# Kernel tuning notes

Hardware: AMD Instinct MI355X
Metric: run time of the kernel (lower is better)

## Reference

```python
import jax, jax.numpy as jnp
import numpy as np
import math

B, S, E = 4, 4096, 1024
NUM_HEADS = 16
D = E // NUM_HEADS  # attention_size = 64


def setup_inputs() -> dict:
    key = jax.random.key(0)
    ks = jax.random.split(key, 7)
    queries = jax.random.normal(ks[0], (B, S, E), dtype=jnp.float32)
    keys = jax.random.normal(ks[1], (B, S, E), dtype=jnp.float32)
    values = jax.random.normal(ks[2], (B, S, E), dtype=jnp.float32)
    mask = jax.random.randint(ks[3], (B, S, S), 0, 2).astype(bool)
    # nn.Linear(E, D, bias=False): weight [D, E], y = x @ W^T
    lim = 1.0 / math.sqrt(E)
    W_q = jax.random.uniform(ks[4], (D, E), jnp.float32, -lim, lim)
    W_k = jax.random.uniform(ks[5], (D, E), jnp.float32, -lim, lim)
    W_v = jax.random.uniform(ks[6], (D, E), jnp.float32, -lim, lim)
    return {"queries": queries, "keys": keys, "values": values, "mask": mask,
            "W_q": W_q, "W_k": W_k, "W_v": W_v}


def reference(queries, keys, values, mask, W_q, W_k, W_v):
    Q = jnp.einsum('bse,de->bsd', queries, W_q)  # [B,S,D]
    K = jnp.einsum('bse,de->bsd', keys, W_k)
    V = jnp.einsum('bse,de->bsd', values, W_v)
    norm = math.sqrt(D)
    scores = jnp.einsum('bqd,bkd->bqk', Q, K) / norm  # [B,S,S]
    scores = jnp.where(mask, jnp.float32(-1e20), scores)
    attn = jax.nn.softmax(scores, axis=2)
    return jnp.einsum('bqk,bkd->bqd', attn, V)  # [B,S,D]
```

## Files before the change

### kernel.cpp

```cpp
#include <hip/hip_runtime.h>
#include <hip/hip_bf16.h>
#include <math.h>

#define NB 4
#define NS 4096
#define NE 1024
#define ND 64

typedef short bf16x8 __attribute__((ext_vector_type(8)));
typedef float f32x4  __attribute__((ext_vector_type(4)));

__device__ unsigned short g_Wb[3 * ND * NE];
__device__ unsigned short g_Qp[NB * NS * ND];
__device__ unsigned short g_Kp[NB * NS * ND];
__device__ unsigned short g_Vt[NB * ND * NS];
__device__ int g_flag;

static __device__ inline unsigned short f2bf(float f) {
    __hip_bfloat16 h = __float2bfloat16(f);
    return *reinterpret_cast<unsigned short*>(&h);
}
static __device__ inline unsigned int f2bf2(float lo, float hi) {
    __hip_bfloat162 h = __float22bfloat162_rn(make_float2(lo, hi));
    return *reinterpret_cast<unsigned int*>(&h);
}
static __device__ inline float bf2f(short s) {
    return __uint_as_float(((unsigned int)(unsigned short)s) << 16);
}

#define AS1 __attribute__((address_space(1)))
#define AS3 __attribute__((address_space(3)))
static __device__ __forceinline__ void gll16(const void* g, void* l) {
    __builtin_amdgcn_global_load_lds((const AS1 void*)g, (AS3 void*)l, 16, 0, 0);
}

__global__ void detect_mask(const unsigned int* __restrict__ mw) {
    __shared__ int found;
    if (threadIdx.x == 0) found = 0;
    __syncthreads();
    int f = 0;
    for (int i = threadIdx.x; i < 4096; i += 256)
        if (mw[i] > 1u) f = 1;
    if (f) atomicOr(&found, 1);
    __syncthreads();
    if (threadIdx.x == 0) g_flag = found;
}

__global__ void prep_w(const float* __restrict__ Wq, const float* __restrict__ Wk,
                       const float* __restrict__ Wv) {
    const int z = blockIdx.x;
    const float* W = (z == 0) ? Wq : (z == 1) ? Wk : Wv;
    unsigned short* o = g_Wb + (size_t)z * (ND * NE);
    const float scale = (z == 0) ? 0.125f : 1.0f;
    int i0 = blockIdx.y * 2048 + threadIdx.x * 8;
    float4 a = *(const float4*)&W[i0];
    float4 b = *(const float4*)&W[i0 + 4];
    ushort4 u0 = { f2bf(a.x * scale), f2bf(a.y * scale), f2bf(a.z * scale), f2bf(a.w * scale) };
    ushort4 u1 = { f2bf(b.x * scale), f2bf(b.y * scale), f2bf(b.z * scale), f2bf(b.w * scale) };
    *(ushort4*)&o[i0]     = u0;
    *(ushort4*)&o[i0 + 4] = u1;
}

__global__ __launch_bounds__(256) void proj_kernel(
    const float* __restrict__ Xq, const float* __restrict__ Xk, const float* __restrict__ Xv)
{
    __shared__ unsigned short Xs[2][64][72];

    const int z = blockIdx.y;
    const float* X = (z == 0) ? Xq : (z == 1) ? Xk : Xv;
    const unsigned short* W = g_Wb + (size_t)z * (ND * NE);

    const int t    = threadIdx.x;
    const int wv   = t >> 6;
    const int lane = t & 63;
    const int quad = lane >> 4;
    const int l16  = lane & 15;
    const int m0   = blockIdx.x * 64;

    const int sr  = t >> 4;
    const int sc4 = (t & 15) * 4;
    const float* Xb = X + (size_t)m0 * NE;

    float4 xr[4][4];

    #pragma unroll
    for (int d = 0; d < 4; ++d)
        #pragma unroll
        for (int p = 0; p < 4; ++p)
            xr[d][p] = *(const float4*)&Xb[(size_t)(sr + p * 16) * NE + d * 64 + sc4];
    #pragma unroll
    for (int p = 0; p < 4; ++p) {
        uint2 u = { f2bf2(xr[0][p].x, xr[0][p].y), f2bf2(xr[0][p].z, xr[0][p].w) };
        *(uint2*)&Xs[0][sr + p * 16][sc4] = u;
    }
    __syncthreads();

    f32x4 acc[4] = {};

    #pragma unroll
    for (int c = 0; c < 16; ++c) {
        if (c + 4 < 16) {
            #pragma unroll
            for (int p = 0; p < 4; ++p)
                xr[c & 3][p] = *(const float4*)&Xb[(size_t)(sr + p * 16) * NE + (c + 4) * 64 + sc4];
        }

        #pragma unroll
        for (int ks = 0; ks < 2; ++ks) {
            bf16x8 a = *(const bf16x8*)&Xs[c & 1][wv * 16 + l16][ks * 32 + quad * 8];
            #pragma unroll
            for (int nt = 0; nt < 4; ++nt) {
                bf16x8 bb = *(const bf16x8*)&W[(size_t)(nt * 16 + l16) * NE + c * 64 + ks * 32 + quad * 8];
                acc[nt] = __builtin_amdgcn_mfma_f32_16x16x32_bf16(a, bb, acc[nt], 0, 0, 0);
            }
        }

        if (c + 1 < 16) {
            #pragma unroll
            for (int p = 0; p < 4; ++p) {
                float4 v = xr[(c + 1) & 3][p];
                uint2 u = { f2bf2(v.x, v.y), f2bf2(v.z, v.w) };
                *(uint2*)&Xs[(c + 1) & 1][sr + p * 16][sc4] = u;
            }
        }
        __syncthreads();
    }

    #pragma unroll
    for (int nt = 0; nt < 4; ++nt)
        #pragma unroll
        for (int r = 0; r < 4; ++r) {
            int m   = m0 + wv * 16 + quad * 4 + r;
            int col = nt * 16 + l16;
            unsigned short u = f2bf(acc[nt][r]);
            if (z == 0)      g_Qp[(size_t)m * ND + col] = u;
            else if (z == 1) g_Kp[(size_t)m * ND + col] = u;
            else             g_Vt[((size_t)(m >> 12) * ND + col) * NS + (m & 4095)] = u;
        }
}

__global__ __launch_bounds__(256) void attn_kernel(
    const void* __restrict__ maskp, float* __restrict__ out)
{
    __shared__ unsigned short KT[2][64 * 64];
    __shared__ unsigned short VT[2][64 * 64];
    __shared__ unsigned char  MR[4][4][1024];
    __shared__ short          Ss[4][16][72];

    const int t    = threadIdx.x;
    const int wv   = t >> 6;
    const int lane = t & 63;
    const int quad = lane >> 4;
    const int l16  = lane & 15;

    const int n    = blockIdx.x;
    const int xcd  = n & 7;
    const int b    = xcd >> 1;
    const int q0   = ((n >> 3) * 2 + (xcd & 1)) * 64;
    const int wq0  = q0 + wv * 16;

    const bool m_u8 = (g_flag != 0);
    const unsigned char* m8  = (const unsigned char*)maskp;
    const int*           m32 = (const int*)maskp;

    const unsigned short* Qrow = g_Qp + ((size_t)b * NS + wq0 + l16) * ND;
    const bf16x8 qf0 = *(const bf16x8*)&Qrow[quad * 8];
    const bf16x8 qf1 = *(const bf16x8*)&Qrow[32 + quad * 8];

    const unsigned short* Kbase = g_Kp + ((size_t)b * NS) * ND;
    const unsigned short* Vbase = g_Vt + (size_t)b * ND * NS;

    const int r8 = lane >> 3;
    const int c8 = lane & 7;
    const int sw = c8 ^ r8;

    const unsigned char* m8base =
        m8 + ((size_t)b * NS + wq0 + (lane >> 2)) * (size_t)NS + (lane & 3) * 16;

    float l_row = 0.0f;
    f32x4 Oacc[4] = {};

    const int rsw = l16 & 7;

    if (m_u8) {
        #pragma unroll
        for (int j = 0; j < 2; ++j) {
            const int row = wv * 16 + j * 8 + r8;
            gll16(Kbase + (size_t)row * 64 + sw * 8, &KT[0][(wv * 16 + j * 8) * 64]);
            gll16(Vbase + (size_t)row * 4096 + sw * 8, &VT[0][(wv * 16 + j * 8) * 64]);
        }
        gll16(m8base, &MR[0][wv][0]);
        gll16(m8base + 64, &MR[1][wv][0]);
        asm volatile("s_waitcnt vmcnt(1)" ::: "memory");
        __builtin_amdgcn_s_barrier();

        #pragma unroll 2
        for (int it = 0; it < 64; ++it) {
            const int buf = it & 1;
            const int k0  = it * 64;

            if (it < 63) {
                const int k1 = k0 + 64;
                #pragma unroll
                for (int j = 0; j < 2; ++j) {
                    const int row = wv * 16 + j * 8 + r8;
                    gll16(Kbase + (size_t)(k1 + row) * 64 + sw * 8,
                          &KT[buf ^ 1][(wv * 16 + j * 8) * 64]);
                    gll16(Vbase + (size_t)row * 4096 + k1 + sw * 8,
                          &VT[buf ^ 1][(wv * 16 + j * 8) * 64]);
                }
            }
            if (it < 62)
                gll16(m8base + (it + 2) * 64, &MR[(it + 2) & 3][wv][0]);

            f32x4 sc[4] = {};
            #pragma unroll
            for (int kt = 0; kt < 4; ++kt) {
                const int row = kt * 16 + l16;
                bf16x8 kf0 = *(const bf16x8*)&KT[buf][row * 64 + ((quad ^ rsw) << 3)];
                bf16x8 kf1 = *(const bf16x8*)&KT[buf][row * 64 + (((4 + quad) ^ rsw) << 3)];
                sc[kt] = __builtin_amdgcn_mfma_f32_16x16x32_bf16(qf0, kf0, sc[kt], 0, 0, 0);
                sc[kt] = __builtin_amdgcn_mfma_f32_16x16x32_bf16(qf1, kf1, sc[kt], 0, 0, 0);
            }

            #pragma unroll
            for (int kt = 0; kt < 4; ++kt)
                #pragma unroll
                for (int r = 0; r < 4; ++r)
                    Ss[wv][quad * 4 + r][kt * 16 + l16] = (short)f2bf(__expf(sc[kt][r]));

            asm volatile("s_waitcnt lgkmcnt(0)" ::: "memory");

            bf16x8 a0 = *(const bf16x8*)&Ss[wv][l16][quad * 8];
            bf16x8 a1 = *(const bf16x8*)&Ss[wv][l16][32 + quad * 8];
            {
                const unsigned char* MRt = &MR[it & 3][wv][0];
                uint2 mm0 = *(const uint2*)&MRt[l16 * 64 + quad * 8];
                uint2 mm1 = *(const uint2*)&MRt[l16 * 64 + 32 + quad * 8];
                #pragma unroll
                for (int j = 0; j < 4; ++j) {
                    a0[j]     = ((mm0.x >> (8 * j)) & 255u) ? (short)0 : a0[j];
                    a0[4 + j] = ((mm0.y >> (8 * j)) & 255u) ? (short)0 : a0[4 + j];
                    a1[j]     = ((mm1.x >> (8 * j)) & 255u) ? (short)0 : a1[j];
                    a1[4 + j] = ((mm1.y >> (8 * j)) & 255u) ? (short)0 : a1[4 + j];
                }
            }
            {
                float ls = 0.0f;
                #pragma unroll
                for (int j = 0; j < 8; ++j) ls += bf2f(a0[j]) + bf2f(a1[j]);
                l_row += ls;
            }
            #pragma unroll
            for (int nt = 0; nt < 4; ++nt) {
                const int row = nt * 16 + l16;
                bf16x8 vf0 = *(const bf16x8*)&VT[buf][row * 64 + ((quad ^ rsw) << 3)];
                bf16x8 vf1 = *(const bf16x8*)&VT[buf][row * 64 + (((4 + quad) ^ rsw) << 3)];
                Oacc[nt] = __builtin_amdgcn_mfma_f32_16x16x32_bf16(a0, vf0, Oacc[nt], 0, 0, 0);
                Oacc[nt] = __builtin_amdgcn_mfma_f32_16x16x32_bf16(a1, vf1, Oacc[nt], 0, 0, 0);
            }

            if (it < 63) {
                if (it < 62) asm volatile("s_waitcnt vmcnt(1)" ::: "memory");
                else         asm volatile("s_waitcnt vmcnt(0)" ::: "memory");
                __builtin_amdgcn_s_barrier();
            }
        }
    } else {
        #pragma unroll
        for (int j = 0; j < 2; ++j) {
            const int row = wv * 16 + j * 8 + r8;
            gll16(Kbase + (size_t)row * 64 + sw * 8, &KT[0][(wv * 16 + j * 8) * 64]);
            gll16(Vbase + (size_t)row * 4096 + sw * 8, &VT[0][(wv * 16 + j * 8) * 64]);
        }
        asm volatile("s_waitcnt vmcnt(0)" ::: "memory");
        __builtin_amdgcn_s_barrier();

        #pragma unroll 2
        for (int it = 0; it < 64; ++it) {
            const int buf = it & 1;
            const int k0  = it * 64;

            if (it < 63) {
                const int k1 = k0 + 64;
                #pragma unroll
                for (int j = 0; j < 2; ++j) {
                    const int row = wv * 16 + j * 8 + r8;
                    gll16(Kbase + (size_t)(k1 + row) * 64 + sw * 8,
                          &KT[buf ^ 1][(wv * 16 + j * 8) * 64]);
                    gll16(Vbase + (size_t)row * 4096 + k1 + sw * 8,
                          &VT[buf ^ 1][(wv * 16 + j * 8) * 64]);
                }
            }

            f32x4 sc[4] = {};
            #pragma unroll
            for (int kt = 0; kt < 4; ++kt) {
                const int row = kt * 16 + l16;
                bf16x8 kf0 = *(const bf16x8*)&KT[buf][row * 64 + ((quad ^ rsw) << 3)];
                bf16x8 kf1 = *(const bf16x8*)&KT[buf][row * 64 + (((4 + quad) ^ rsw) << 3)];
                sc[kt] = __builtin_amdgcn_mfma_f32_16x16x32_bf16(qf0, kf0, sc[kt], 0, 0, 0);
                sc[kt] = __builtin_amdgcn_mfma_f32_16x16x32_bf16(qf1, kf1, sc[kt], 0, 0, 0);
            }

            #pragma unroll
            for (int r = 0; r < 4; ++r) {
                size_t mrow = ((size_t)b * NS + (wq0 + quad * 4 + r)) * (size_t)NS + k0;
                #pragma unroll
                for (int kt = 0; kt < 4; ++kt) {
                    int mv = m32[mrow + kt * 16 + l16];
                    float p = mv ? 0.0f : __expf(sc[kt][r]);
                    Ss[wv][quad * 4 + r][kt * 16 + l16] = (short)f2bf(p);
                }
            }

            asm volatile("s_waitcnt lgkmcnt(0)" ::: "memory");

            bf16x8 a0 = *(const bf16x8*)&Ss[wv][l16][quad * 8];
            bf16x8 a1 = *(const bf16x8*)&Ss[wv][l16][32 + quad * 8];
            {
                float ls = 0.0f;
                #pragma unroll
                for (int j = 0; j < 8; ++j) ls += bf2f(a0[j]) + bf2f(a1[j]);
                l_row += ls;
            }
            #pragma unroll
            for (int nt = 0; nt < 4; ++nt) {
                const int row = nt * 16 + l16;
                bf16x8 vf0 = *(const bf16x8*)&VT[buf][row * 64 + ((quad ^ rsw) << 3)];
                bf16x8 vf1 = *(const bf16x8*)&VT[buf][row * 64 + (((4 + quad) ^ rsw) << 3)];
                Oacc[nt] = __builtin_amdgcn_mfma_f32_16x16x32_bf16(a0, vf0, Oacc[nt], 0, 0, 0);
                Oacc[nt] = __builtin_amdgcn_mfma_f32_16x16x32_bf16(a1, vf1, Oacc[nt], 0, 0, 0);
            }

            if (it < 63) {
                asm volatile("s_waitcnt vmcnt(0)" ::: "memory");
                __builtin_amdgcn_s_barrier();
            }
        }
    }

    l_row += __shfl_xor(l_row, 16);
    l_row += __shfl_xor(l_row, 32);
    const float inv = 1.0f / l_row;

    #pragma unroll
    for (int r = 0; r < 4; ++r) {
        const float invm = __shfl(inv, quad * 4 + r);
        const int m = wq0 + quad * 4 + r;
        #pragma unroll
        for (int nt = 0; nt < 4; ++nt)
            out[((size_t)b * NS + m) * ND + nt * 16 + l16] = Oacc[nt][r] * invm;
    }
}

extern "C" void kernel_launch(void* const* d_in, const int* in_sizes, int n_in,
                              void* d_out, int out_size, void* d_ws, size_t ws_size,
                              hipStream_t stream) {
    const float* queries = (const float*)d_in[0];
    const float* keys    = (const float*)d_in[1];
    const float* values  = (const float*)d_in[2];
    const void*  mask    = d_in[3];
    const float* Wq      = (const float*)d_in[4];
    const float* Wk      = (const float*)d_in[5];
    const float* Wv      = (const float*)d_in[6];
    float* out = (float*)d_out;

    hipLaunchKernelGGL(detect_mask, dim3(1), dim3(256), 0, stream,
                       (const unsigned int*)mask);
    hipLaunchKernelGGL(prep_w, dim3(3, 32), dim3(256), 0, stream, Wq, Wk, Wv);
    hipLaunchKernelGGL(proj_kernel, dim3((NB * NS) / 64, 3), dim3(256), 0, stream,
                       queries, keys, values);
    hipLaunchKernelGGL(attn_kernel, dim3(NS / 64 * NB), dim3(256), 0, stream,
                       mask, out);
}
```

Baseline: 583.3 us.

## Split attention keys across two blocks, add merge kernel, coalesce projection stores

The attention grid doubles to 512 blocks, each handling half of the key range (split-K). Unnormalized partial outputs and row sums go to global scratch, and a new merge kernel adds them and normalizes. This is meant to fill more CUs and raise per-CU occupancy, since the old grid had only one block per CU. The projection epilogue now transposes through LDS so global writes are wide and coalesced, and s_setprio is raised around the MFMA sections. The cost is an extra kernel launch plus a write and read of fp32 partial results.

```diff
diff --git a/kernel.cpp b/kernel.cpp
--- a/kernel.cpp
+++ b/kernel.cpp
@@ -14,6 +14,8 @@
 __device__ unsigned short g_Qp[NB * NS * ND];
 __device__ unsigned short g_Kp[NB * NS * ND];
 __device__ unsigned short g_Vt[NB * ND * NS];
+__device__ float g_Po[NB * 64 * 2 * 64 * ND];
+__device__ float g_Pl[NB * 64 * 2 * 64];
 __device__ int g_flag;
 
 static __device__ inline unsigned short f2bf(float f) {
@@ -32,6 +34,11 @@
 #define AS3 __attribute__((address_space(3)))
 static __device__ __forceinline__ void gll16(const void* g, void* l) {
     __builtin_amdgcn_global_load_lds((const AS1 void*)g, (AS3 void*)l, 16, 0, 0);
+}
+
+static __device__ __forceinline__ void lds_barrier() {
+    asm volatile("s_waitcnt lgkmcnt(0)" ::: "memory");
+    __builtin_amdgcn_s_barrier();
 }
 
 __global__ void detect_mask(const unsigned int* __restrict__ mw) {
@@ -93,7 +100,7 @@
         uint2 u = { f2bf2(xr[0][p].x, xr[0][p].y), f2bf2(xr[0][p].z, xr[0][p].w) };
         *(uint2*)&Xs[0][sr + p * 16][sc4] = u;
     }
-    __syncthreads();
+    lds_barrier();
 
     f32x4 acc[4] = {};
 
@@ -123,24 +130,46 @@
                 *(uint2*)&Xs[(c + 1) & 1][sr + p * 16][sc4] = u;
             }
         }
-        __syncthreads();
-    }
-
-    #pragma unroll
-    for (int nt = 0; nt < 4; ++nt)
-        #pragma unroll
-        for (int r = 0; r < 4; ++r) {
-            int m   = m0 + wv * 16 + quad * 4 + r;
-            int col = nt * 16 + l16;
-            unsigned short u = f2bf(acc[nt][r]);
-            if (z == 0)      g_Qp[(size_t)m * ND + col] = u;
-            else if (z == 1) g_Kp[(size_t)m * ND + col] = u;
-            else             g_Vt[((size_t)(m >> 12) * ND + col) * NS + (m & 4095)] = u;
-        }
+        lds_barrier();
+    }
+
+    unsigned short (*T)[68] = (unsigned short(*)[68])&Xs[0][0][0];
+
+    if (z == 2) {
+        #pragma unroll
+        for (int nt = 0; nt < 4; ++nt)
+            #pragma unroll
+            for (int r = 0; r < 4; ++r)
+                T[nt * 16 + l16][wv * 16 + quad * 4 + r] = f2bf(acc[nt][r]);
+    } else {
+        #pragma unroll
+        for (int nt = 0; nt < 4; ++nt)
+            #pragma unroll
+            for (int r = 0; r < 4; ++r)
+                T[wv * 16 + quad * 4 + r][nt * 16 + l16] = f2bf(acc[nt][r]);
+    }
+    lds_barrier();
+
+    {
+        const int dr  = t >> 2;
+        const int c16 = (t & 3) * 16;
+        uint4 u0 = *(const uint4*)&T[dr][c16];
+        uint4 u1 = *(const uint4*)&T[dr][c16 + 8];
+        if (z == 2) {
+            const int bb = m0 >> 12, s0 = m0 & 4095;
+            unsigned short* dst = g_Vt + ((size_t)bb * ND + dr) * NS + s0 + c16;
+            *(uint4*)&dst[0] = u0;
+            *(uint4*)&dst[8] = u1;
+        } else {
+            unsigned short* dst = (z == 0 ? g_Qp : g_Kp) + (size_t)(m0 + dr) * ND + c16;
+            *(uint4*)&dst[0] = u0;
+            *(uint4*)&dst[8] = u1;
+        }
+    }
 }
 
 __global__ __launch_bounds__(256) void attn_kernel(
-    const void* __restrict__ maskp, float* __restrict__ out)
+    const void* __restrict__ maskp)
 {
     __shared__ unsigned short KT[2][64 * 64];
     __shared__ unsigned short VT[2][64 * 64];
@@ -156,8 +185,11 @@
     const int n    = blockIdx.x;
     const int xcd  = n & 7;
     const int b    = xcd >> 1;
-    const int q0   = ((n >> 3) * 2 + (xcd & 1)) * 64;
+    const int kh   = xcd & 1;
+    const int qt   = n >> 3;
+    const int q0   = qt * 64;
     const int wq0  = q0 + wv * 16;
+    const int koff = kh * 2048;
 
     const bool m_u8 = (g_flag != 0);
     const unsigned char* m8  = (const unsigned char*)maskp;
@@ -174,8 +206,8 @@
     const int c8 = lane & 7;
     const int sw = c8 ^ r8;
 
-    const unsigned char* m8base =
-        m8 + ((size_t)b * NS + wq0 + (lane >> 2)) * (size_t)NS + (lane & 3) * 16;
+    const unsigned char* m8k =
+        m8 + ((size_t)b * NS + wq0 + (lane >> 2)) * (size_t)NS + koff + (lane & 3) * 16;
 
     float l_row = 0.0f;
     f32x4 Oacc[4] = {};
@@ -186,34 +218,35 @@
         #pragma unroll
         for (int j = 0; j < 2; ++j) {
             const int row = wv * 16 + j * 8 + r8;
-            gll16(Kbase + (size_t)row * 64 + sw * 8, &KT[0][(wv * 16 + j * 8) * 64]);
-            gll16(Vbase + (size_t)row * 4096 + sw * 8, &VT[0][(wv * 16 + j * 8) * 64]);
-        }
-        gll16(m8base, &MR[0][wv][0]);
-        gll16(m8base + 64, &MR[1][wv][0]);
+            gll16(Kbase + ((size_t)koff + row) * 64 + sw * 8, &KT[0][(wv * 16 + j * 8) * 64]);
+            gll16(Vbase + (size_t)row * NS + koff + sw * 8, &VT[0][(wv * 16 + j * 8) * 64]);
+        }
+        gll16(m8k, &MR[0][wv][0]);
+        gll16(m8k + 64, &MR[1][wv][0]);
         asm volatile("s_waitcnt vmcnt(1)" ::: "memory");
         __builtin_amdgcn_s_barrier();
 
         #pragma unroll 2
-        for (int it = 0; it < 64; ++it) {
+        for (int it = 0; it < 32; ++it) {
             const int buf = it & 1;
-            const int k0  = it * 64;
-
-            if (it < 63) {
+            const int k0  = koff + it * 64;
+
+            if (it < 31) {
                 const int k1 = k0 + 64;
                 #pragma unroll
                 for (int j = 0; j < 2; ++j) {
                     const int row = wv * 16 + j * 8 + r8;
                     gll16(Kbase + (size_t)(k1 + row) * 64 + sw * 8,
                           &KT[buf ^ 1][(wv * 16 + j * 8) * 64]);
-                    gll16(Vbase + (size_t)row * 4096 + k1 + sw * 8,
+                    gll16(Vbase + (size_t)row * NS + k1 + sw * 8,
                           &VT[buf ^ 1][(wv * 16 + j * 8) * 64]);
                 }
             }
-            if (it < 62)
-                gll16(m8base + (it + 2) * 64, &MR[(it + 2) & 3][wv][0]);
+            if (it < 30)
+                gll16(m8k + (it + 2) * 64, &MR[(it + 2) & 3][wv][0]);
 
             f32x4 sc[4] = {};
+            __builtin_amdgcn_s_setprio(1);
             #pragma unroll
             for (int kt = 0; kt < 4; ++kt) {
                 const int row = kt * 16 + l16;
@@ -222,6 +255,7 @@
                 sc[kt] = __builtin_amdgcn_mfma_f32_16x16x32_bf16(qf0, kf0, sc[kt], 0, 0, 0);
                 sc[kt] = __builtin_amdgcn_mfma_f32_16x16x32_bf16(qf1, kf1, sc[kt], 0, 0, 0);
             }
+            __builtin_amdgcn_s_setprio(0);
 
             #pragma unroll
             for (int kt = 0; kt < 4; ++kt)
@@ -251,6 +285,7 @@
                 for (int j = 0; j < 8; ++j) ls += bf2f(a0[j]) + bf2f(a1[j]);
                 l_row += ls;
             }
+            __builtin_amdgcn_s_setprio(1);
             #pragma unroll
             for (int nt = 0; nt < 4; ++nt) {
                 const int row = nt * 16 + l16;
@@ -259,9 +294,10 @@
                 Oacc[nt] = __builtin_amdgcn_mfma_f32_16x16x32_bf16(a0, vf0, Oacc[nt], 0, 0, 0);
                 Oacc[nt] = __builtin_amdgcn_mfma_f32_16x16x32_bf16(a1, vf1, Oacc[nt], 0, 0, 0);
             }
-
-            if (it < 63) {
-                if (it < 62) asm volatile("s_waitcnt vmcnt(1)" ::: "memory");
+            __builtin_amdgcn_s_setprio(0);
+
+            if (it < 31) {
+                if (it < 30) asm volatile("s_waitcnt vmcnt(1)" ::: "memory");
                 else         asm volatile("s_waitcnt vmcnt(0)" ::: "memory");
                 __builtin_amdgcn_s_barrier();
             }
@@ -270,25 +306,25 @@
         #pragma unroll
         for (int j = 0; j < 2; ++j) {
             const int row = wv * 16 + j * 8 + r8;
-            gll16(Kbase + (size_t)row * 64 + sw * 8, &KT[0][(wv * 16 + j * 8) * 64]);
-            gll16(Vbase + (size_t)row * 4096 + sw * 8, &VT[0][(wv * 16 + j * 8) * 64]);
+            gll16(Kbase + ((size_t)koff + row) * 64 + sw * 8, &KT[0][(wv * 16 + j * 8) * 64]);
+            gll16(Vbase + (size_t)row * NS + koff + sw * 8, &VT[0][(wv * 16 + j * 8) * 64]);
         }
         asm volatile("s_waitcnt vmcnt(0)" ::: "memory");
         __builtin_amdgcn_s_barrier();
 
         #pragma unroll 2
-        for (int it = 0; it < 64; ++it) {
+        for (int it = 0; it < 32; ++it) {
             const int buf = it & 1;
-            const int k0  = it * 64;
-
-            if (it < 63) {
+            const int k0  = koff + it * 64;
+
+            if (it < 31) {
                 const int k1 = k0 + 64;
                 #pragma unroll
                 for (int j = 0; j < 2; ++j) {
                     const int row = wv * 16 + j * 8 + r8;
                     gll16(Kbase + (size_t)(k1 + row) * 64 + sw * 8,
                           &KT[buf ^ 1][(wv * 16 + j * 8) * 64]);
-                    gll16(Vbase + (size_t)row * 4096 + k1 + sw * 8,
+                    gll16(Vbase + (size_t)row * NS + k1 + sw * 8,
                           &VT[buf ^ 1][(wv * 16 + j * 8) * 64]);
                 }
             }
@@ -333,7 +369,7 @@
                 Oacc[nt] = __builtin_amdgcn_mfma_f32_16x16x32_bf16(a1, vf1, Oacc[nt], 0, 0, 0);
             }
 
-            if (it < 63) {
+            if (it < 31) {
                 asm volatile("s_waitcnt vmcnt(0)" ::: "memory");
                 __builtin_amdgcn_s_barrier();
             }
@@ -342,16 +378,33 @@
 
     l_row += __shfl_xor(l_row, 16);
     l_row += __shfl_xor(l_row, 32);
-    const float inv = 1.0f / l_row;
-
+
+    float* po = g_Po + ((((size_t)b * 64 + qt) * 2 + kh) * 64) * 64;
     #pragma unroll
     for (int r = 0; r < 4; ++r) {
-        const float invm = __shfl(inv, quad * 4 + r);
-        const int m = wq0 + quad * 4 + r;
+        const int ql = wv * 16 + quad * 4 + r;
         #pragma unroll
         for (int nt = 0; nt < 4; ++nt)
-            out[((size_t)b * NS + m) * ND + nt * 16 + l16] = Oacc[nt][r] * invm;
-    }
+            po[(size_t)ql * 64 + nt * 16 + l16] = Oacc[nt][r];
+    }
+    if (quad == 0)
+        g_Pl[(((size_t)b * 64 + qt) * 2 + kh) * 64 + wv * 16 + l16] = l_row;
+}
+
+__global__ __launch_bounds__(256) void merge_kernel(float* __restrict__ out) {
+    const int tid = blockIdx.x * 256 + threadIdx.x;
+    const int r   = tid >> 4;
+    const int d4  = (tid & 15) * 4;
+    const int b = r >> 12, s = r & 4095, qt = s >> 6, ql = s & 63;
+    const size_t base = ((size_t)b * 64 + qt) * 2;
+    const float* p0 = g_Po + ((base + 0) * 64 + ql) * 64 + d4;
+    const float* p1 = g_Po + ((base + 1) * 64 + ql) * 64 + d4;
+    f32x4 a = *(const f32x4*)p0;
+    f32x4 c = *(const f32x4*)p1;
+    float l = g_Pl[(base + 0) * 64 + ql] + g_Pl[(base + 1) * 64 + ql];
+    float inv = 1.0f / l;
+    f32x4 o = (a + c) * inv;
+    *(f32x4*)&out[(size_t)r * ND + d4] = o;
 }
 
 extern "C" void kernel_launch(void* const* d_in, const int* in_sizes, int n_in,
@@ -371,6 +424,6 @@
     hipLaunchKernelGGL(prep_w, dim3(3, 32), dim3(256), 0, stream, Wq, Wk, Wv);
     hipLaunchKernelGGL(proj_kernel, dim3((NB * NS) / 64, 3), dim3(256), 0, stream,
                        queries, keys, values);
-    hipLaunchKernelGGL(attn_kernel, dim3(NS / 64 * NB), dim3(256), 0, stream,
-                       mask, out);
-}
+    hipLaunchKernelGGL(attn_kernel, dim3(512), dim3(256), 0, stream, mask);
+    hipLaunchKernelGGL(merge_kernel, dim3(1024), dim3(256), 0, stream, out);
+}
```

After: 536.7 us. 1.09x faster.
